# Performance work log

Hardware: AMD Instinct MI355X
Metric: run time of the kernel (lower is better)

Reference implementation:

```python
import jax, jax.numpy as jnp
import numpy as np
from jax.ops import segment_sum, segment_max

N, E, F_IN, H1, H2, HEADS, OUT, G = 50000, 800000, 64, 64, 64, 4, 32, 500

def setup_inputs() -> dict:
    key = jax.random.key(0)
    ks = jax.random.split(key, 12)
    x = jax.random.normal(ks[0], (N, F_IN), dtype=jnp.float32)
    edge_index = jax.random.randint(ks[1], (2, E), 0, N, dtype=jnp.int64)
    batch = jnp.sort(jax.random.randint(ks[2], (N,), 0, G, dtype=jnp.int64))
    def glorot(k, shape):
        fan = shape[0] + shape[-1]
        return jax.random.uniform(k, shape, jnp.float32, -1.0, 1.0) * jnp.sqrt(6.0 / fan)
    return {
        "x": x,
        "edge_index": edge_index,
        "batch": batch,
        "gcn_W": glorot(ks[3], (F_IN, H1)),
        "gcn_b": jnp.zeros((H1,), jnp.float32),
        "gat_W": glorot(ks[4], (H1, HEADS * H2)),
        "att_src": glorot(ks[5], (HEADS, H2)),
        "att_dst": glorot(ks[6], (HEADS, H2)),
        "gat_b": jnp.zeros((HEADS * H2,), jnp.float32),
        "out_W": glorot(ks[7], (HEADS * H2, OUT)),
        "out_b": jnp.zeros((OUT,), jnp.float32),
    }

def reference(x, edge_index, batch, gcn_W, gcn_b, gat_W, att_src, att_dst, gat_b, out_W, out_b):
    n = x.shape[0]
    loop = jnp.arange(n)
    # edges with self-loops: src (j) -> dst (i), PyG convention
    src = jnp.concatenate([edge_index[0], loop])
    dst = jnp.concatenate([edge_index[1], loop])

    # ---- GCNConv: symmetric normalized scatter-add ----
    h = x @ gcn_W                                            # [N, H1]
    deg = segment_sum(jnp.ones_like(dst, dtype=h.dtype), dst, num_segments=n)
    dinv = jnp.where(deg > 0, jax.lax.rsqrt(deg), 0.0)       # deg^{-1/2}
    norm = dinv[src] * dinv[dst]                             # [E']
    h = segment_sum(norm[:, None] * h[src], dst, num_segments=n) + gcn_b
    h = jax.nn.relu(h)

    # ---- GATConv: per-edge attention + segment softmax over dst ----
    g = (h @ gat_W).reshape(n, HEADS, H2)                    # [N, H, C]
    a_s = jnp.einsum('nhc,hc->nh', g, att_src)               # [N, H]
    a_d = jnp.einsum('nhc,hc->nh', g, att_dst)
    e = jax.nn.leaky_relu(a_s[src] + a_d[dst], 0.2)          # [E', H]
    m = segment_max(e, dst, num_segments=n)                  # every node has a self-loop
    e = jnp.exp(e - m[dst])
    denom = segment_sum(e, dst, num_segments=n)
    alpha = e / denom[dst]                                   # [E', H]
    agg = segment_sum(alpha[:, :, None] * g[src], dst, num_segments=n)  # [N, H, C]
    z = jax.nn.relu(agg.reshape(n, HEADS * H2) + gat_b)

    # ---- global mean pool over graphs + output linear ----
    cnt = segment_sum(jnp.ones((n,), z.dtype), batch, num_segments=G)
    pooled = segment_sum(z, batch, num_segments=G) / jnp.maximum(cnt, 1.0)[:, None]
    return pooled @ out_W + out_b
```

## Files before the change

### kernel.cpp

```cpp
#include <hip/hip_runtime.h>
#include <math.h>

#define NN 50000
#define NE 800000
#define NEP (NE + NN)
#define NGRAPH 500
#define NOUT 32
#define NBLK 196

typedef _Float16 half4 __attribute__((ext_vector_type(4)));
typedef _Float16 half2v __attribute__((ext_vector_type(2)));

__device__ __forceinline__ float lrelu(float x) { return x > 0.f ? x : 0.2f * x; }
__device__ __forceinline__ half2v bch2(float f) { return __builtin_bit_cast(half2v, f); }

__device__ __forceinline__ unsigned fkey(float f) {
    unsigned b = __float_as_uint(f);
    return (b & 0x80000000u) ? ~b : (b | 0x80000000u);
}
__device__ __forceinline__ float funkey(unsigned k) {
    unsigned b = (k & 0x80000000u) ? (k & 0x7fffffffu) : ~k;
    return __uint_as_float(b);
}


__global__ void k_count(const int* __restrict__ dst, int* __restrict__ cnt,
                        int* __restrict__ pos) {
    int e = blockIdx.x * blockDim.x + threadIdx.x;
    if (e < NE) pos[e] = atomicAdd(&cnt[dst[e]], 1);
}

__global__ __launch_bounds__(256) void k_scan1(const int* __restrict__ cnt, int* __restrict__ bsum,
                                               float* __restrict__ pool, float* __restrict__ cnt_g) {
    __shared__ int buf[256];
    int gid = blockIdx.x * 256 + threadIdx.x;
    int v = (gid < NN) ? (cnt[gid] + 1) : 0;
    buf[threadIdx.x] = v;
    for (int j = gid; j < NGRAPH * 256; j += NBLK * 256) pool[j] = 0.f;
    if (gid < NGRAPH) cnt_g[gid] = 0.f;
    __syncthreads();
    for (int off = 128; off; off >>= 1) {
        if (threadIdx.x < off) buf[threadIdx.x] += buf[threadIdx.x + off];
        __syncthreads();
    }
    if (threadIdx.x == 0) bsum[blockIdx.x] = buf[0];
}

__global__ __launch_bounds__(256) void k_scan3(const int* __restrict__ cnt,
                                               const int* __restrict__ bsum,
                                               int* __restrict__ row_ptr,
                                               float* __restrict__ dinv,
                                               int* __restrict__ col) {
    __shared__ int sb[256];
    __shared__ int buf[256];
    int tid = threadIdx.x;
    int bv = (tid < NBLK) ? bsum[tid] : 0;
    sb[tid] = bv;
    __syncthreads();
    for (int off = 1; off < 256; off <<= 1) {
        int t = (tid >= off) ? sb[tid - off] : 0;
        __syncthreads();
        sb[tid] += t;
        __syncthreads();
    }
    int blockoff = (blockIdx.x == 0) ? 0 : sb[blockIdx.x - 1];
    int i = blockIdx.x * 256 + tid;
    int v = (i < NN) ? (cnt[i] + 1) : 0;
    buf[tid] = v;
    __syncthreads();
    for (int off = 1; off < 256; off <<= 1) {
        int t = (tid >= off) ? buf[tid - off] : 0;
        __syncthreads();
        buf[tid] += t;
        __syncthreads();
    }
    if (i < NN) {
        int rp = blockoff + buf[tid] - v;
        row_ptr[i] = rp;
        dinv[i] = rsqrtf((float)(cnt[i] + 1));
        col[rp] = i;
    }
    if (i == 0) row_ptr[NN] = NEP;
}

__global__ void k_fill(const int* __restrict__ src, const int* __restrict__ dst,
                       const int* __restrict__ row_ptr, const int* __restrict__ pos,
                       int* __restrict__ col) {
    int idx = blockIdx.x * blockDim.x + threadIdx.x;
    if (idx < NE) {
        int d = dst[idx];
        col[row_ptr[d] + 1 + pos[idx]] = src[idx];
    }
}


__global__ __launch_bounds__(256) void k_gemm64(const float* __restrict__ A,
                                                const float* __restrict__ B,
                                                _Float16* __restrict__ C16, int n) {
    __shared__ float Bs[64 * 64];
    __shared__ float As[64 * 68];
    int tid = threadIdx.x;
    int rb = blockIdx.x * 64;
    for (int i = tid; i < 1024; i += 256) ((float4*)Bs)[i] = ((const float4*)B)[i];
    for (int i = tid; i < 1024; i += 256) {
        int r = i >> 4, c = i & 15;
        int row = rb + r; if (row >= n) row = n - 1;
        ((float4*)As)[r * 17 + c] = ((const float4*)A)[(size_t)row * 16 + c];
    }
    __syncthreads();
    int lane = tid & 63, wv = tid >> 6;
    int fl = lane & 15, sub = lane >> 4;
    int r0 = wv * 16 + sub * 4;
    const float4* Bs4 = (const float4*)Bs;
    float4 acc0 = {0,0,0,0}, acc1 = {0,0,0,0}, acc2 = {0,0,0,0}, acc3 = {0,0,0,0};
#pragma unroll 4
    for (int k = 0; k < 64; ++k) {
        float4 b4 = Bs4[k * 16 + fl];
        float a0 = As[(r0 + 0) * 68 + k];
        float a1 = As[(r0 + 1) * 68 + k];
        float a2 = As[(r0 + 2) * 68 + k];
        float a3 = As[(r0 + 3) * 68 + k];
        acc0.x += a0 * b4.x; acc0.y += a0 * b4.y; acc0.z += a0 * b4.z; acc0.w += a0 * b4.w;
        acc1.x += a1 * b4.x; acc1.y += a1 * b4.y; acc1.z += a1 * b4.z; acc1.w += a1 * b4.w;
        acc2.x += a2 * b4.x; acc2.y += a2 * b4.y; acc2.z += a2 * b4.z; acc2.w += a2 * b4.w;
        acc3.x += a3 * b4.x; acc3.y += a3 * b4.y; acc3.z += a3 * b4.z; acc3.w += a3 * b4.w;
    }
    int row = rb + r0;
    half4 h0, h1, h2, h3;
    h0.x=(_Float16)acc0.x; h0.y=(_Float16)acc0.y; h0.z=(_Float16)acc0.z; h0.w=(_Float16)acc0.w;
    h1.x=(_Float16)acc1.x; h1.y=(_Float16)acc1.y; h1.z=(_Float16)acc1.z; h1.w=(_Float16)acc1.w;
    h2.x=(_Float16)acc2.x; h2.y=(_Float16)acc2.y; h2.z=(_Float16)acc2.z; h2.w=(_Float16)acc2.w;
    h3.x=(_Float16)acc3.x; h3.y=(_Float16)acc3.y; h3.z=(_Float16)acc3.z; h3.w=(_Float16)acc3.w;
    if (row + 0 < n) ((half4*)(C16 + (size_t)(row + 0) * 64))[fl] = h0;
    if (row + 1 < n) ((half4*)(C16 + (size_t)(row + 1) * 64))[fl] = h1;
    if (row + 2 < n) ((half4*)(C16 + (size_t)(row + 2) * 64))[fl] = h2;
    if (row + 3 < n) ((half4*)(C16 + (size_t)(row + 3) * 64))[fl] = h3;
}


__global__ void k_uv(const float* __restrict__ gat_W, const float* __restrict__ att_src,
                     const float* __restrict__ att_dst, float* __restrict__ UV) {
    int idx = blockIdx.x * blockDim.x + threadIdx.x;
    if (idx >= 512) return;
    int f = idx >> 3, o = idx & 7, h = o & 3;
    const float* av = (o < 4) ? att_src : att_dst;
    float s = 0.f;
#pragma unroll 8
    for (int c = 0; c < 64; ++c) s += gat_W[f * 256 + h * 64 + c] * av[h * 64 + c];
    UV[idx] = s;
}


__global__ void k_w16t(const float* __restrict__ W, _Float16* __restrict__ W16T) {
    int idx = blockIdx.x * blockDim.x + threadIdx.x;
    if (idx >= 64 * 256) return;
    int c = idx >> 6, f = idx & 63;
    W16T[idx] = (_Float16)W[f * 256 + c];
}


__global__ __launch_bounds__(256) void k_gcn_agg(const _Float16* __restrict__ hx16,
                                                 const int* __restrict__ row_ptr,
                                                 const int* __restrict__ col,
                                                 const float* __restrict__ dinv,
                                                 const float* __restrict__ bias,
                                                 const float* __restrict__ UV,
                                                 _Float16* __restrict__ h16,
                                                 float* __restrict__ a_s,
                                                 float* __restrict__ a_d) {
    int wid = (blockIdx.x * blockDim.x + threadIdx.x) >> 6;
    int lane = threadIdx.x & 63;
    if (wid >= NN) return;
    int sub = lane >> 4;
    int fl  = lane & 15;
    int s0 = row_ptr[wid], s1 = row_ptr[wid + 1];
    float di = dinv[wid];
    const half4* hx4 = (const half4*)hx16;
    float ax = 0.f, ay = 0.f, az = 0.f, aw = 0.f;
    int k = s0 + sub;
    for (; k + 4 < s1; k += 8) {
        int sA = col[k], sB = col[k + 4];
        float wA = dinv[sA] * di, wB = dinv[sB] * di;
        half4 vA = hx4[(size_t)sA * 16 + fl];
        half4 vB = hx4[(size_t)sB * 16 + fl];
        ax += wA * (float)vA.x + wB * (float)vB.x;
        ay += wA * (float)vA.y + wB * (float)vB.y;
        az += wA * (float)vA.z + wB * (float)vB.z;
        aw += wA * (float)vA.w + wB * (float)vB.w;
    }
    if (k < s1) {
        int s = col[k];
        float w = dinv[s] * di;
        half4 v = hx4[(size_t)s * 16 + fl];
        ax += w * (float)v.x; ay += w * (float)v.y;
        az += w * (float)v.z; aw += w * (float)v.w;
    }
    ax += __shfl_xor(ax, 16); ax += __shfl_xor(ax, 32);
    ay += __shfl_xor(ay, 16); ay += __shfl_xor(ay, 32);
    az += __shfl_xor(az, 16); az += __shfl_xor(az, 32);
    aw += __shfl_xor(aw, 16); aw += __shfl_xor(aw, 32);
    float4 bb = ((const float4*)bias)[fl];
    float zx = fmaxf(ax + bb.x, 0.f);
    float zy = fmaxf(ay + bb.y, 0.f);
    float zz = fmaxf(az + bb.z, 0.f);
    float zw = fmaxf(aw + bb.w, 0.f);
    if (sub == 0) {
        half4 z;
        z.x = (_Float16)zx; z.y = (_Float16)zy; z.z = (_Float16)zz; z.w = (_Float16)zw;
        ((half4*)(h16 + (size_t)wid * 64))[fl] = z;
    }
    int f0 = fl * 4;
    float ps = zx * UV[(f0 + 0) * 8 + sub] + zy * UV[(f0 + 1) * 8 + sub]
             + zz * UV[(f0 + 2) * 8 + sub] + zw * UV[(f0 + 3) * 8 + sub];
    float pd = zx * UV[(f0 + 0) * 8 + 4 + sub] + zy * UV[(f0 + 1) * 8 + 4 + sub]
             + zz * UV[(f0 + 2) * 8 + 4 + sub] + zw * UV[(f0 + 3) * 8 + 4 + sub];
    ps += __shfl_xor(ps, 1); pd += __shfl_xor(pd, 1);
    ps += __shfl_xor(ps, 2); pd += __shfl_xor(pd, 2);
    ps += __shfl_xor(ps, 4); pd += __shfl_xor(pd, 4);
    ps += __shfl_xor(ps, 8); pd += __shfl_xor(pd, 8);
    if (fl == 0) {
        a_s[wid * 4 + sub] = ps;
        a_d[wid * 4 + sub] = pd;
    }
}


__global__ __launch_bounds__(256) void k_gmax(const float* __restrict__ a_s,
                                              unsigned* __restrict__ gmaxU) {
    __shared__ unsigned sm[4];
    int tid = threadIdx.x;
    if (tid < 4) sm[tid] = 0u;
    __syncthreads();
    float mx = -1e30f, my = -1e30f, mz = -1e30f, mw = -1e30f;
    int stride = gridDim.x * 256;
    for (int n = blockIdx.x * 256 + tid; n < NN; n += stride) {
        float4 v = ((const float4*)a_s)[n];
        mx = fmaxf(mx, v.x); my = fmaxf(my, v.y);
        mz = fmaxf(mz, v.z); mw = fmaxf(mw, v.w);
    }
    atomicMax(&sm[0], fkey(mx)); atomicMax(&sm[1], fkey(my));
    atomicMax(&sm[2], fkey(mz)); atomicMax(&sm[3], fkey(mw));
    __syncthreads();
    if (tid < 4) atomicMax(&gmaxU[tid], sm[tid]);
}


__global__ __launch_bounds__(256) void k_gat_h(const _Float16* __restrict__ h16,
                                               const float* __restrict__ a_s,
                                               const float* __restrict__ a_d,
                                               const int* __restrict__ row_ptr,
                                               const int* __restrict__ col,
                                               const unsigned* __restrict__ gmaxU,
                                               _Float16* __restrict__ aggH) {
    int tid = threadIdx.x;
    int wv = tid >> 6, lane = tid & 63;
    int wid = blockIdx.x * 4 + wv;
    int hh = lane >> 4;
    int fl = lane & 15;

    int s0 = row_ptr[wid], s1 = row_ptr[wid + 1];
    float adsel = a_d[wid * 4 + hh];
    float M = lrelu(funkey(gmaxU[hh]) + adsel);
    const half4* h4 = (const half4*)h16;

    float t = 1e-30f;
    float ax = 0.f, ay = 0.f, az = 0.f, aw = 0.f;

    int k = s0;
    for (; k + 7 < s1; k += 8) {
        int i0 = col[k], i1 = col[k + 1], i2 = col[k + 2], i3 = col[k + 3];
        int i4 = col[k + 4], i5 = col[k + 5], i6 = col[k + 6], i7 = col[k + 7];
        half4 g0 = h4[(size_t)i0 * 16 + fl];
        half4 g1 = h4[(size_t)i1 * 16 + fl];
        half4 g2 = h4[(size_t)i2 * 16 + fl];
        half4 g3 = h4[(size_t)i3 * 16 + fl];
        half4 g4v = h4[(size_t)i4 * 16 + fl];
        half4 g5v = h4[(size_t)i5 * 16 + fl];
        half4 g6 = h4[(size_t)i6 * 16 + fl];
        half4 g7 = h4[(size_t)i7 * 16 + fl];
        float w0 = __expf(lrelu(a_s[i0 * 4 + hh] + adsel) - M);
        float w1 = __expf(lrelu(a_s[i1 * 4 + hh] + adsel) - M);
        float w2 = __expf(lrelu(a_s[i2 * 4 + hh] + adsel) - M);
        float w3 = __expf(lrelu(a_s[i3 * 4 + hh] + adsel) - M);
        float w4 = __expf(lrelu(a_s[i4 * 4 + hh] + adsel) - M);
        float w5 = __expf(lrelu(a_s[i5 * 4 + hh] + adsel) - M);
        float w6 = __expf(lrelu(a_s[i6 * 4 + hh] + adsel) - M);
        float w7 = __expf(lrelu(a_s[i7 * 4 + hh] + adsel) - M);
        t += ((w0 + w1) + (w2 + w3)) + ((w4 + w5) + (w6 + w7));
        ax += w0 * (float)g0.x + w1 * (float)g1.x + w2 * (float)g2.x + w3 * (float)g3.x
            + w4 * (float)g4v.x + w5 * (float)g5v.x + w6 * (float)g6.x + w7 * (float)g7.x;
        ay += w0 * (float)g0.y + w1 * (float)g1.y + w2 * (float)g2.y + w3 * (float)g3.y
            + w4 * (float)g4v.y + w5 * (float)g5v.y + w6 * (float)g6.y + w7 * (float)g7.y;
        az += w0 * (float)g0.z + w1 * (float)g1.z + w2 * (float)g2.z + w3 * (float)g3.z
            + w4 * (float)g4v.z + w5 * (float)g5v.z + w6 * (float)g6.z + w7 * (float)g7.z;
        aw += w0 * (float)g0.w + w1 * (float)g1.w + w2 * (float)g2.w + w3 * (float)g3.w
            + w4 * (float)g4v.w + w5 * (float)g5v.w + w6 * (float)g6.w + w7 * (float)g7.w;
    }
    for (; k + 3 < s1; k += 4) {
        int i0 = col[k], i1 = col[k + 1], i2 = col[k + 2], i3 = col[k + 3];
        half4 g0 = h4[(size_t)i0 * 16 + fl];
        half4 g1 = h4[(size_t)i1 * 16 + fl];
        half4 g2 = h4[(size_t)i2 * 16 + fl];
        half4 g3 = h4[(size_t)i3 * 16 + fl];
        float w0 = __expf(lrelu(a_s[i0 * 4 + hh] + adsel) - M);
        float w1 = __expf(lrelu(a_s[i1 * 4 + hh] + adsel) - M);
        float w2 = __expf(lrelu(a_s[i2 * 4 + hh] + adsel) - M);
        float w3 = __expf(lrelu(a_s[i3 * 4 + hh] + adsel) - M);
        t += (w0 + w1) + (w2 + w3);
        ax += w0 * (float)g0.x + w1 * (float)g1.x + w2 * (float)g2.x + w3 * (float)g3.x;
        ay += w0 * (float)g0.y + w1 * (float)g1.y + w2 * (float)g2.y + w3 * (float)g3.y;
        az += w0 * (float)g0.z + w1 * (float)g1.z + w2 * (float)g2.z + w3 * (float)g3.z;
        aw += w0 * (float)g0.w + w1 * (float)g1.w + w2 * (float)g2.w + w3 * (float)g3.w;
    }
    for (; k < s1; ++k) {
        int s = col[k];
        half4 gv = h4[(size_t)s * 16 + fl];
        float w = __expf(lrelu(a_s[s * 4 + hh] + adsel) - M);
        t += w;
        ax += w * (float)gv.x; ay += w * (float)gv.y;
        az += w * (float)gv.z; aw += w * (float)gv.w;
    }
    float r = 1.f / t;
    half4 o;
    o.x = (_Float16)(ax * r); o.y = (_Float16)(ay * r);
    o.z = (_Float16)(az * r); o.w = (_Float16)(aw * r);
    ((half4*)(aggH + (size_t)wid * 256))[lane] = o;
}


__global__ __launch_bounds__(256) void k_post2(const _Float16* __restrict__ aggH,
                                               const _Float16* __restrict__ W16T,
                                               const float* __restrict__ gat_b,
                                               const int* __restrict__ batch,
                                               float* __restrict__ pool,
                                               float* __restrict__ cnt_g) {
    int tid = threadIdx.x;
    int lane = tid & 63;
    int wv = __builtin_amdgcn_readfirstlane(tid >> 6);
    int h = blockIdx.y;
    int c = h * 64 + lane;
    const float4* wp = (const float4*)(W16T + (size_t)c * 64);
    float4 Wb[8];
#pragma unroll
    for (int i = 0; i < 8; ++i) Wb[i] = wp[i];
    float gb = gat_b[c];

    int rbeg = (blockIdx.x * 4 + wv) * 32;
    int rend = rbeg + 32; if (rend > NN) rend = NN;

    float psum = 0.f;
    int curb = -1, rcnt = 0;
#pragma unroll 2
    for (int row = rbeg; row < rend; ++row) {
        int b = batch[row];
        if (b != curb) {
            if (curb >= 0) {
                atomicAdd(&pool[(size_t)curb * 256 + c], psum);
                if (h == 0 && lane == 0) atomicAdd(&cnt_g[curb], (float)rcnt);
            }
            psum = 0.f; rcnt = 0; curb = b;
        }
        const float4* ap = (const float4*)(aggH + (size_t)row * 256 + h * 64);
        float4 Ab[8];
#pragma unroll
        for (int i = 0; i < 8; ++i) Ab[i] = ap[i];
        float ac0 = 0.f, ac1 = 0.f, ac2 = 0.f, ac3 = 0.f;
#pragma unroll
        for (int i = 0; i < 8; ++i) {
            ac0 = __builtin_amdgcn_fdot2(bch2(Ab[i].x), bch2(Wb[i].x), ac0, false);
            ac1 = __builtin_amdgcn_fdot2(bch2(Ab[i].y), bch2(Wb[i].y), ac1, false);
            ac2 = __builtin_amdgcn_fdot2(bch2(Ab[i].z), bch2(Wb[i].z), ac2, false);
            ac3 = __builtin_amdgcn_fdot2(bch2(Ab[i].w), bch2(Wb[i].w), ac3, false);
        }
        float acc = (ac0 + ac1) + (ac2 + ac3);
        psum += fmaxf(acc + gb, 0.f);
        ++rcnt;
    }
    if (curb >= 0) {
        atomicAdd(&pool[(size_t)curb * 256 + c], psum);
        if (h == 0 && lane == 0) atomicAdd(&cnt_g[curb], (float)rcnt);
    }
}


__global__ void k_out(const float* __restrict__ pool, const float* __restrict__ cnt_g,
                      const float* __restrict__ W, const float* __restrict__ b,
                      float* __restrict__ out) {
    int idx = blockIdx.x * blockDim.x + threadIdx.x;
    if (idx >= NGRAPH * NOUT) return;
    int gg = idx >> 5, o = idx & 31;
    float c = cnt_g[gg];
    c = c > 1.f ? c : 1.f;
    float rinv = 1.f / c;
    const float* p = pool + (size_t)gg * 256;
    float acc = 0.f;
#pragma unroll 8
    for (int f = 0; f < 256; ++f) acc += p[f] * W[f * 32 + o];
    out[idx] = acc * rinv + b[o];
}


extern "C" void kernel_launch(void* const* d_in, const int* in_sizes, int n_in,
                              void* d_out, int out_size, void* d_ws, size_t ws_size,
                              hipStream_t stream) {
    const float* x       = (const float*)d_in[0];
    const int*   eidx    = (const int*)d_in[1];
    const int*   batch   = (const int*)d_in[2];
    const float* gcn_W   = (const float*)d_in[3];
    const float* gcn_b   = (const float*)d_in[4];
    const float* gat_W   = (const float*)d_in[5];
    const float* att_src = (const float*)d_in[6];
    const float* att_dst = (const float*)d_in[7];
    const float* gat_b   = (const float*)d_in[8];
    const float* out_W   = (const float*)d_in[9];
    const float* out_b   = (const float*)d_in[10];
    float* out = (float*)d_out;

    const int* src = eidx;
    const int* dst = eidx + NE;

    size_t off = 0;
    auto carve = [&](size_t bytes) -> char* {
        char* p = (char*)d_ws + off;
        off += (bytes + 255) & ~(size_t)255;
        return p;
    };
    int*      cnt     = (int*)carve(NN * sizeof(int));
    int*      pos     = (int*)carve((size_t)NE * sizeof(int));
    int*      row_ptr = (int*)carve((NN + 1) * sizeof(int));
    int*      bsum    = (int*)carve(256 * sizeof(int));
    int*      colb    = (int*)carve((size_t)NEP * sizeof(int));
    float*    dinv    = (float*)carve(NN * sizeof(float));
    _Float16* hx16    = (_Float16*)carve((size_t)NN * 64 * sizeof(_Float16));
    _Float16* h16     = (_Float16*)carve((size_t)NN * 64 * sizeof(_Float16));
    _Float16* aggH16  = (_Float16*)carve((size_t)NN * 256 * sizeof(_Float16));
    float*    a_s     = (float*)carve((size_t)NN * 4 * sizeof(float));
    float*    a_d     = (float*)carve((size_t)NN * 4 * sizeof(float));
    float*    UV      = (float*)carve(64 * 8 * sizeof(float));
    _Float16* W16T    = (_Float16*)carve(64 * 256 * sizeof(_Float16));
    unsigned* gmaxU   = (unsigned*)carve(4 * sizeof(unsigned));
    float*    pool    = (float*)carve((size_t)NGRAPH * 256 * sizeof(float));
    float*    cnt_g   = (float*)carve(NGRAPH * sizeof(float));

    hipMemsetAsync(cnt, 0, NN * sizeof(int), stream);
    hipMemsetAsync(gmaxU, 0, 4 * sizeof(unsigned), stream);

    k_count<<<(NE + 255) / 256, 256, 0, stream>>>(dst, cnt, pos);
    k_scan1<<<NBLK, 256, 0, stream>>>(cnt, bsum, pool, cnt_g);
    k_scan3<<<NBLK, 256, 0, stream>>>(cnt, bsum, row_ptr, dinv, colb);
    k_fill<<<(NE + 255) / 256, 256, 0, stream>>>(src, dst, row_ptr, pos, colb);

    k_uv<<<2, 256, 0, stream>>>(gat_W, att_src, att_dst, UV);
    k_w16t<<<64, 256, 0, stream>>>(gat_W, W16T);

    k_gemm64<<<(NN + 63) / 64, 256, 0, stream>>>(x, gcn_W, hx16, NN);
    k_gcn_agg<<<(NN * 64 + 255) / 256, 256, 0, stream>>>(hx16, row_ptr, colb, dinv, gcn_b,
                                                         UV, h16, a_s, a_d);

    k_gmax<<<128, 256, 0, stream>>>(a_s, gmaxU);
    k_gat_h<<<NN / 4, 256, 0, stream>>>(h16, a_s, a_d, row_ptr, colb, gmaxU, aggH16);

    k_post2<<<dim3(391, 4), 256, 0, stream>>>(aggH16, W16T, gat_b, batch, pool, cnt_g);

    k_out<<<(NGRAPH * NOUT + 255) / 256, 256, 0, stream>>>(pool, cnt_g, out_W, out_b, out);
}
```

Before: 326.6 us.

## Pre-scale GCN features by dinv and split GAT edges across lane slots

The GEMM epilogue now multiplies each row by dinv[src], so the GCN aggregation no longer gathers dinv per edge and applies dinv[dst] once after the reduction. The GCN loop is unrolled to four independent gathers per slot. The GAT kernel changes from one head per 16-lane slot walking every edge to four slots each taking every fourth edge and computing all four heads. It loads a_s as a float4 and reduces across slots with shuffles at the end. This cuts redundant per-edge index and feature loads, at the cost of more registers, extra exp work per lane and fp16 rounding of the pre-scaled values.

```diff
diff --git a/kernel.cpp b/kernel.cpp
--- a/kernel.cpp
+++ b/kernel.cpp
@@ -96,6 +96,7 @@
 
 __global__ __launch_bounds__(256) void k_gemm64(const float* __restrict__ A,
                                                 const float* __restrict__ B,
+                                                const float* __restrict__ dinv,
                                                 _Float16* __restrict__ C16, int n) {
     __shared__ float Bs[64 * 64];
     __shared__ float As[64 * 68];
@@ -126,11 +127,15 @@
         acc3.x += a3 * b4.x; acc3.y += a3 * b4.y; acc3.z += a3 * b4.z; acc3.w += a3 * b4.w;
     }
     int row = rb + r0;
+    float d0 = dinv[row + 0 < n ? row + 0 : n - 1];
+    float d1 = dinv[row + 1 < n ? row + 1 : n - 1];
+    float d2 = dinv[row + 2 < n ? row + 2 : n - 1];
+    float d3 = dinv[row + 3 < n ? row + 3 : n - 1];
     half4 h0, h1, h2, h3;
-    h0.x=(_Float16)acc0.x; h0.y=(_Float16)acc0.y; h0.z=(_Float16)acc0.z; h0.w=(_Float16)acc0.w;
-    h1.x=(_Float16)acc1.x; h1.y=(_Float16)acc1.y; h1.z=(_Float16)acc1.z; h1.w=(_Float16)acc1.w;
-    h2.x=(_Float16)acc2.x; h2.y=(_Float16)acc2.y; h2.z=(_Float16)acc2.z; h2.w=(_Float16)acc2.w;
-    h3.x=(_Float16)acc3.x; h3.y=(_Float16)acc3.y; h3.z=(_Float16)acc3.z; h3.w=(_Float16)acc3.w;
+    h0.x=(_Float16)(acc0.x*d0); h0.y=(_Float16)(acc0.y*d0); h0.z=(_Float16)(acc0.z*d0); h0.w=(_Float16)(acc0.w*d0);
+    h1.x=(_Float16)(acc1.x*d1); h1.y=(_Float16)(acc1.y*d1); h1.z=(_Float16)(acc1.z*d1); h1.w=(_Float16)(acc1.w*d1);
+    h2.x=(_Float16)(acc2.x*d2); h2.y=(_Float16)(acc2.y*d2); h2.z=(_Float16)(acc2.z*d2); h2.w=(_Float16)(acc2.w*d2);
+    h3.x=(_Float16)(acc3.x*d3); h3.y=(_Float16)(acc3.y*d3); h3.z=(_Float16)(acc3.z*d3); h3.w=(_Float16)(acc3.w*d3);
     if (row + 0 < n) ((half4*)(C16 + (size_t)(row + 0) * 64))[fl] = h0;
     if (row + 1 < n) ((half4*)(C16 + (size_t)(row + 1) * 64))[fl] = h1;
     if (row + 2 < n) ((half4*)(C16 + (size_t)(row + 2) * 64))[fl] = h2;
@@ -159,7 +164,7 @@
 }
 
 
-__global__ __launch_bounds__(256) void k_gcn_agg(const _Float16* __restrict__ hx16,
+__global__ __launch_bounds__(256) void k_gcn_agg(const _Float16* __restrict__ hxs16,
                                                  const int* __restrict__ row_ptr,
                                                  const int* __restrict__ col,
                                                  const float* __restrict__ dinv,
@@ -171,56 +176,55 @@
     int wid = (blockIdx.x * blockDim.x + threadIdx.x) >> 6;
     int lane = threadIdx.x & 63;
     if (wid >= NN) return;
-    int sub = lane >> 4;
-    int fl  = lane & 15;
+    int slot = lane >> 4;
+    int fl   = lane & 15;
     int s0 = row_ptr[wid], s1 = row_ptr[wid + 1];
     float di = dinv[wid];
-    const half4* hx4 = (const half4*)hx16;
+    const half4* hx4 = (const half4*)hxs16;
     float ax = 0.f, ay = 0.f, az = 0.f, aw = 0.f;
-    int k = s0 + sub;
-    for (; k + 4 < s1; k += 8) {
-        int sA = col[k], sB = col[k + 4];
-        float wA = dinv[sA] * di, wB = dinv[sB] * di;
-        half4 vA = hx4[(size_t)sA * 16 + fl];
-        half4 vB = hx4[(size_t)sB * 16 + fl];
-        ax += wA * (float)vA.x + wB * (float)vB.x;
-        ay += wA * (float)vA.y + wB * (float)vB.y;
-        az += wA * (float)vA.z + wB * (float)vB.z;
-        aw += wA * (float)vA.w + wB * (float)vB.w;
-    }
-    if (k < s1) {
-        int s = col[k];
-        float w = dinv[s] * di;
-        half4 v = hx4[(size_t)s * 16 + fl];
-        ax += w * (float)v.x; ay += w * (float)v.y;
-        az += w * (float)v.z; aw += w * (float)v.w;
+    int k = s0 + slot;
+    for (; k + 12 < s1; k += 16) {
+        int i0 = col[k], i1 = col[k + 4], i2 = col[k + 8], i3 = col[k + 12];
+        half4 v0 = hx4[(size_t)i0 * 16 + fl];
+        half4 v1 = hx4[(size_t)i1 * 16 + fl];
+        half4 v2 = hx4[(size_t)i2 * 16 + fl];
+        half4 v3 = hx4[(size_t)i3 * 16 + fl];
+        ax += ((float)v0.x + (float)v1.x) + ((float)v2.x + (float)v3.x);
+        ay += ((float)v0.y + (float)v1.y) + ((float)v2.y + (float)v3.y);
+        az += ((float)v0.z + (float)v1.z) + ((float)v2.z + (float)v3.z);
+        aw += ((float)v0.w + (float)v1.w) + ((float)v2.w + (float)v3.w);
+    }
+    for (; k < s1; k += 4) {
+        half4 v = hx4[(size_t)col[k] * 16 + fl];
+        ax += (float)v.x; ay += (float)v.y;
+        az += (float)v.z; aw += (float)v.w;
     }
     ax += __shfl_xor(ax, 16); ax += __shfl_xor(ax, 32);
     ay += __shfl_xor(ay, 16); ay += __shfl_xor(ay, 32);
     az += __shfl_xor(az, 16); az += __shfl_xor(az, 32);
     aw += __shfl_xor(aw, 16); aw += __shfl_xor(aw, 32);
     float4 bb = ((const float4*)bias)[fl];
-    float zx = fmaxf(ax + bb.x, 0.f);
-    float zy = fmaxf(ay + bb.y, 0.f);
-    float zz = fmaxf(az + bb.z, 0.f);
-    float zw = fmaxf(aw + bb.w, 0.f);
-    if (sub == 0) {
+    float zx = fmaxf(ax * di + bb.x, 0.f);
+    float zy = fmaxf(ay * di + bb.y, 0.f);
+    float zz = fmaxf(az * di + bb.z, 0.f);
+    float zw = fmaxf(aw * di + bb.w, 0.f);
+    if (slot == 0) {
         half4 z;
         z.x = (_Float16)zx; z.y = (_Float16)zy; z.z = (_Float16)zz; z.w = (_Float16)zw;
         ((half4*)(h16 + (size_t)wid * 64))[fl] = z;
     }
     int f0 = fl * 4;
-    float ps = zx * UV[(f0 + 0) * 8 + sub] + zy * UV[(f0 + 1) * 8 + sub]
-             + zz * UV[(f0 + 2) * 8 + sub] + zw * UV[(f0 + 3) * 8 + sub];
-    float pd = zx * UV[(f0 + 0) * 8 + 4 + sub] + zy * UV[(f0 + 1) * 8 + 4 + sub]
-             + zz * UV[(f0 + 2) * 8 + 4 + sub] + zw * UV[(f0 + 3) * 8 + 4 + sub];
+    float ps = zx * UV[(f0 + 0) * 8 + slot] + zy * UV[(f0 + 1) * 8 + slot]
+             + zz * UV[(f0 + 2) * 8 + slot] + zw * UV[(f0 + 3) * 8 + slot];
+    float pd = zx * UV[(f0 + 0) * 8 + 4 + slot] + zy * UV[(f0 + 1) * 8 + 4 + slot]
+             + zz * UV[(f0 + 2) * 8 + 4 + slot] + zw * UV[(f0 + 3) * 8 + 4 + slot];
     ps += __shfl_xor(ps, 1); pd += __shfl_xor(pd, 1);
     ps += __shfl_xor(ps, 2); pd += __shfl_xor(pd, 2);
     ps += __shfl_xor(ps, 4); pd += __shfl_xor(pd, 4);
     ps += __shfl_xor(ps, 8); pd += __shfl_xor(pd, 8);
     if (fl == 0) {
-        a_s[wid * 4 + sub] = ps;
-        a_d[wid * 4 + sub] = pd;
+        a_s[wid * 4 + slot] = ps;
+        a_d[wid * 4 + slot] = pd;
     }
 }
 
@@ -255,75 +259,76 @@
     int tid = threadIdx.x;
     int wv = tid >> 6, lane = tid & 63;
     int wid = blockIdx.x * 4 + wv;
-    int hh = lane >> 4;
+    int slot = lane >> 4;
     int fl = lane & 15;
 
     int s0 = row_ptr[wid], s1 = row_ptr[wid + 1];
-    float adsel = a_d[wid * 4 + hh];
-    float M = lrelu(funkey(gmaxU[hh]) + adsel);
+    float4 ad4 = ((const float4*)a_d)[wid];
+    float M0 = lrelu(funkey(gmaxU[0]) + ad4.x);
+    float M1 = lrelu(funkey(gmaxU[1]) + ad4.y);
+    float M2 = lrelu(funkey(gmaxU[2]) + ad4.z);
+    float M3 = lrelu(funkey(gmaxU[3]) + ad4.w);
     const half4* h4 = (const half4*)h16;
-
-    float t = 1e-30f;
-    float ax = 0.f, ay = 0.f, az = 0.f, aw = 0.f;
-
-    int k = s0;
-    for (; k + 7 < s1; k += 8) {
-        int i0 = col[k], i1 = col[k + 1], i2 = col[k + 2], i3 = col[k + 3];
-        int i4 = col[k + 4], i5 = col[k + 5], i6 = col[k + 6], i7 = col[k + 7];
-        half4 g0 = h4[(size_t)i0 * 16 + fl];
-        half4 g1 = h4[(size_t)i1 * 16 + fl];
-        half4 g2 = h4[(size_t)i2 * 16 + fl];
-        half4 g3 = h4[(size_t)i3 * 16 + fl];
-        half4 g4v = h4[(size_t)i4 * 16 + fl];
-        half4 g5v = h4[(size_t)i5 * 16 + fl];
-        half4 g6 = h4[(size_t)i6 * 16 + fl];
-        half4 g7 = h4[(size_t)i7 * 16 + fl];
-        float w0 = __expf(lrelu(a_s[i0 * 4 + hh] + adsel) - M);
-        float w1 = __expf(lrelu(a_s[i1 * 4 + hh] + adsel) - M);
-        float w2 = __expf(lrelu(a_s[i2 * 4 + hh] + adsel) - M);
-        float w3 = __expf(lrelu(a_s[i3 * 4 + hh] + adsel) - M);
-        float w4 = __expf(lrelu(a_s[i4 * 4 + hh] + adsel) - M);
-        float w5 = __expf(lrelu(a_s[i5 * 4 + hh] + adsel) - M);
-        float w6 = __expf(lrelu(a_s[i6 * 4 + hh] + adsel) - M);
-        float w7 = __expf(lrelu(a_s[i7 * 4 + hh] + adsel) - M);
-        t += ((w0 + w1) + (w2 + w3)) + ((w4 + w5) + (w6 + w7));
-        ax += w0 * (float)g0.x + w1 * (float)g1.x + w2 * (float)g2.x + w3 * (float)g3.x
-            + w4 * (float)g4v.x + w5 * (float)g5v.x + w6 * (float)g6.x + w7 * (float)g7.x;
-        ay += w0 * (float)g0.y + w1 * (float)g1.y + w2 * (float)g2.y + w3 * (float)g3.y
-            + w4 * (float)g4v.y + w5 * (float)g5v.y + w6 * (float)g6.y + w7 * (float)g7.y;
-        az += w0 * (float)g0.z + w1 * (float)g1.z + w2 * (float)g2.z + w3 * (float)g3.z
-            + w4 * (float)g4v.z + w5 * (float)g5v.z + w6 * (float)g6.z + w7 * (float)g7.z;
-        aw += w0 * (float)g0.w + w1 * (float)g1.w + w2 * (float)g2.w + w3 * (float)g3.w
-            + w4 * (float)g4v.w + w5 * (float)g5v.w + w6 * (float)g6.w + w7 * (float)g7.w;
-    }
-    for (; k + 3 < s1; k += 4) {
-        int i0 = col[k], i1 = col[k + 1], i2 = col[k + 2], i3 = col[k + 3];
-        half4 g0 = h4[(size_t)i0 * 16 + fl];
-        half4 g1 = h4[(size_t)i1 * 16 + fl];
-        half4 g2 = h4[(size_t)i2 * 16 + fl];
-        half4 g3 = h4[(size_t)i3 * 16 + fl];
-        float w0 = __expf(lrelu(a_s[i0 * 4 + hh] + adsel) - M);
-        float w1 = __expf(lrelu(a_s[i1 * 4 + hh] + adsel) - M);
-        float w2 = __expf(lrelu(a_s[i2 * 4 + hh] + adsel) - M);
-        float w3 = __expf(lrelu(a_s[i3 * 4 + hh] + adsel) - M);
-        t += (w0 + w1) + (w2 + w3);
-        ax += w0 * (float)g0.x + w1 * (float)g1.x + w2 * (float)g2.x + w3 * (float)g3.x;
-        ay += w0 * (float)g0.y + w1 * (float)g1.y + w2 * (float)g2.y + w3 * (float)g3.y;
-        az += w0 * (float)g0.z + w1 * (float)g1.z + w2 * (float)g2.z + w3 * (float)g3.z;
-        aw += w0 * (float)g0.w + w1 * (float)g1.w + w2 * (float)g2.w + w3 * (float)g3.w;
-    }
-    for (; k < s1; ++k) {
-        int s = col[k];
-        half4 gv = h4[(size_t)s * 16 + fl];
-        float w = __expf(lrelu(a_s[s * 4 + hh] + adsel) - M);
-        t += w;
-        ax += w * (float)gv.x; ay += w * (float)gv.y;
-        az += w * (float)gv.z; aw += w * (float)gv.w;
-    }
-    float r = 1.f / t;
+    const float4* as4 = (const float4*)a_s;
+
+    float t0 = 1e-30f, t1 = 1e-30f, t2 = 1e-30f, t3 = 1e-30f;
+    float4 A0 = {0,0,0,0}, A1 = {0,0,0,0}, A2 = {0,0,0,0}, A3 = {0,0,0,0};
+
+    int k = s0 + slot;
+    for (; k + 4 < s1; k += 8) {
+        int ia = col[k], ib = col[k + 4];
+        float4 ea = as4[ia];
+        float4 eb = as4[ib];
+        half4 va = h4[(size_t)ia * 16 + fl];
+        half4 vb = h4[(size_t)ib * 16 + fl];
+        float wa0 = __expf(lrelu(ea.x + ad4.x) - M0);
+        float wa1 = __expf(lrelu(ea.y + ad4.y) - M1);
+        float wa2 = __expf(lrelu(ea.z + ad4.z) - M2);
+        float wa3 = __expf(lrelu(ea.w + ad4.w) - M3);
+        float wb0 = __expf(lrelu(eb.x + ad4.x) - M0);
+        float wb1 = __expf(lrelu(eb.y + ad4.y) - M1);
+        float wb2 = __expf(lrelu(eb.z + ad4.z) - M2);
+        float wb3 = __expf(lrelu(eb.w + ad4.w) - M3);
+        t0 += wa0 + wb0; t1 += wa1 + wb1; t2 += wa2 + wb2; t3 += wa3 + wb3;
+        float vax = (float)va.x, vay = (float)va.y, vaz = (float)va.z, vaw = (float)va.w;
+        float vbx = (float)vb.x, vby = (float)vb.y, vbz = (float)vb.z, vbw = (float)vb.w;
+        A0.x += wa0 * vax + wb0 * vbx; A0.y += wa0 * vay + wb0 * vby;
+        A0.z += wa0 * vaz + wb0 * vbz; A0.w += wa0 * vaw + wb0 * vbw;
+        A1.x += wa1 * vax + wb1 * vbx; A1.y += wa1 * vay + wb1 * vby;
+        A1.z += wa1 * vaz + wb1 * vbz; A1.w += wa1 * vaw + wb1 * vbw;
+        A2.x += wa2 * vax + wb2 * vbx; A2.y += wa2 * vay + wb2 * vby;
+        A2.z += wa2 * vaz + wb2 * vbz; A2.w += wa2 * vaw + wb2 * vbw;
+        A3.x += wa3 * vax + wb3 * vbx; A3.y += wa3 * vay + wb3 * vby;
+        A3.z += wa3 * vaz + wb3 * vbz; A3.w += wa3 * vaw + wb3 * vbw;
+    }
+    if (k < s1) {
+        int ia = col[k];
+        float4 ea = as4[ia];
+        half4 va = h4[(size_t)ia * 16 + fl];
+        float wa0 = __expf(lrelu(ea.x + ad4.x) - M0);
+        float wa1 = __expf(lrelu(ea.y + ad4.y) - M1);
+        float wa2 = __expf(lrelu(ea.z + ad4.z) - M2);
+        float wa3 = __expf(lrelu(ea.w + ad4.w) - M3);
+        t0 += wa0; t1 += wa1; t2 += wa2; t3 += wa3;
+        float vax = (float)va.x, vay = (float)va.y, vaz = (float)va.z, vaw = (float)va.w;
+        A0.x += wa0 * vax; A0.y += wa0 * vay; A0.z += wa0 * vaz; A0.w += wa0 * vaw;
+        A1.x += wa1 * vax; A1.y += wa1 * vay; A1.z += wa1 * vaz; A1.w += wa1 * vaw;
+        A2.x += wa2 * vax; A2.y += wa2 * vay; A2.z += wa2 * vaz; A2.w += wa2 * vaw;
+        A3.x += wa3 * vax; A3.y += wa3 * vay; A3.z += wa3 * vaz; A3.w += wa3 * vaw;
+    }
+#define REDX(x) x += __shfl_xor(x, 16); x += __shfl_xor(x, 32);
+    REDX(t0) REDX(t1) REDX(t2) REDX(t3)
+    REDX(A0.x) REDX(A0.y) REDX(A0.z) REDX(A0.w)
+    REDX(A1.x) REDX(A1.y) REDX(A1.z) REDX(A1.w)
+    REDX(A2.x) REDX(A2.y) REDX(A2.z) REDX(A2.w)
+    REDX(A3.x) REDX(A3.y) REDX(A3.z) REDX(A3.w)
+#undef REDX
+    float rsel = slot == 0 ? t0 : slot == 1 ? t1 : slot == 2 ? t2 : t3;
+    float4 Asel = slot == 0 ? A0 : slot == 1 ? A1 : slot == 2 ? A2 : A3;
+    float r = 1.f / rsel;
     half4 o;
-    o.x = (_Float16)(ax * r); o.y = (_Float16)(ay * r);
-    o.z = (_Float16)(az * r); o.w = (_Float16)(aw * r);
+    o.x = (_Float16)(Asel.x * r); o.y = (_Float16)(Asel.y * r);
+    o.z = (_Float16)(Asel.z * r); o.w = (_Float16)(Asel.w * r);
     ((half4*)(aggH + (size_t)wid * 256))[lane] = o;
 }
 
@@ -453,7 +458,7 @@
     k_uv<<<2, 256, 0, stream>>>(gat_W, att_src, att_dst, UV);
     k_w16t<<<64, 256, 0, stream>>>(gat_W, W16T);
 
-    k_gemm64<<<(NN + 63) / 64, 256, 0, stream>>>(x, gcn_W, hx16, NN);
+    k_gemm64<<<(NN + 63) / 64, 256, 0, stream>>>(x, gcn_W, dinv, hx16, NN);
     k_gcn_agg<<<(NN * 64 + 255) / 256, 256, 0, stream>>>(hx16, row_ptr, colb, dinv, gcn_b,
                                                          UV, h16, a_s, a_d);
 
```

Result: faster. 317.5 us (-2.8%).
